# Kernel tuning notes

Measured on AMD Instinct MI355X. Metric: run time of the kernel, lower is better.

## Reference

```python
import jax, jax.numpy as jnp
import numpy as np

N_NODES = 100000
N_EDGES = 1600000
IN_DIM = 512
HID = 64
OUT_DIM = 5


def _gcn_conv(x, row, col, w, W, b, n_nodes):
    """PyG GCNConv: h = x @ W; out[col] += norm * h[row]; out += b.
    norm = deg^-1/2[row] * w * deg^-1/2[col], deg from edge weights scattered on col,
    with self-loops (weight 1) already appended by caller."""
    h = x @ W  # [N, F_out]
    deg = jax.ops.segment_sum(w, col, num_segments=n_nodes)  # [N]
    dinv = jnp.where(deg > 0, jax.lax.rsqrt(deg), 0.0)
    norm = dinv[row] * w * dinv[col]  # [E']
    msg = h[row] * norm[:, None]  # [E', F_out] edge-wise gather + scale
    out = jax.ops.segment_sum(msg, col, num_segments=n_nodes)  # scatter-add
    return out + b


def setup_inputs() -> dict:
    key = jax.random.key(0)
    ks = jax.random.split(key, 10)
    x = jax.random.normal(ks[0], (N_NODES, IN_DIM), dtype=jnp.float32)
    edge_index = jax.random.randint(ks[1], (2, N_EDGES), 0, N_NODES, dtype=jnp.int32)
    edge_attr = jax.random.uniform(ks[2], (N_EDGES,), dtype=jnp.float32)
    # Glorot-ish init for params
    W1 = jax.random.normal(ks[3], (IN_DIM, HID), dtype=jnp.float32) * (1.0 / np.sqrt(IN_DIM))
    b1 = jnp.zeros((HID,), dtype=jnp.float32)
    W2 = jax.random.normal(ks[4], (HID, HID), dtype=jnp.float32) * (1.0 / np.sqrt(HID))
    b2 = jnp.zeros((HID,), dtype=jnp.float32)
    Wfc = jax.random.normal(ks[5], (HID, OUT_DIM), dtype=jnp.float32) * (1.0 / np.sqrt(HID))
    bfc = jnp.zeros((OUT_DIM,), dtype=jnp.float32)
    return {"x": x, "edge_index": edge_index, "edge_attr": edge_attr,
            "W1": W1, "b1": b1, "W2": W2, "b2": b2, "Wfc": Wfc, "bfc": bfc}


def reference(x, edge_index, edge_attr, W1, b1, W2, b2, Wfc, bfc):
    n = x.shape[0]
    loop = jnp.arange(n, dtype=edge_index.dtype)
    row = jnp.concatenate([edge_index[0], loop])  # source nodes + self-loops
    col = jnp.concatenate([edge_index[1], loop])  # target nodes + self-loops
    w = jnp.concatenate([edge_attr, jnp.ones((n,), dtype=edge_attr.dtype)])
    h = jax.nn.relu(_gcn_conv(x, row, col, w, W1, b1, n))
    # dropout(p=0.5) is identity in eval/reference mode
    h = jax.nn.relu(_gcn_conv(h, row, col, w, W2, b2, n))
    return h @ Wfc + bfc
```

## Files before the change

kernel.cpp:

```cpp
#include <hip/hip_runtime.h>

#define HID 64
#define OUTD 5
#define BCAP 16384
#define PART_CHUNK 4096
#define CSTRIDE 16

typedef __attribute__((ext_vector_type(8))) short bf16x8;
typedef __attribute__((ext_vector_type(4))) float f32x4;

__device__ inline void split_bf16(float x, short& hi, short& lo) {
    unsigned u = __float_as_uint(x);
    unsigned h = u >> 16;
    float hf = __uint_as_float(h << 16);
    float lof = x - hf;
    unsigned l = __float_as_uint(lof) >> 16;
    hi = (short)h; lo = (short)l;
}

__device__ inline ushort f2bf(float x) {
    unsigned u = __float_as_uint(x);
    u += 0x7fffu + ((u >> 16) & 1u);
    return (ushort)(u >> 16);
}

__global__ void k_prep(const float* __restrict__ W1, const float* __restrict__ W2,
                       short* __restrict__ w1hi, short* __restrict__ w1lo,
                       short* __restrict__ w2hi, short* __restrict__ w2lo,
                       int* __restrict__ gcursor, int nbuck,
                       int* __restrict__ binCnt, int* __restrict__ binCur) {
    int gid = blockIdx.x * blockDim.x + threadIdx.x;
    if (gid < nbuck) gcursor[gid * CSTRIDE] = 0;
    if (gid < 64) { binCnt[gid * CSTRIDE] = 0; binCur[gid * CSTRIDE] = 0; }
    if (gid >= 32768 + 4096) return;
    int which = (gid >= 32768);
    int g = which ? gid - 32768 : gid;
    const float* W = which ? W2 : W1;
    short* ph = which ? w2hi : w1hi;
    short* pl = which ? w2lo : w1lo;
    int b = g & 7, lane = (g >> 3) & 63, c = (g >> 9) & 3, s = g >> 11;
    int k = s * 32 + 8 * (lane >> 4) + b;
    int j = c * 16 + (lane & 15);
    float x = W[k * 64 + j];
    short hi, lo; split_bf16(x, hi, lo);
    ph[g] = hi; pl[g] = lo;
}

__device__ inline void gemm1_body(const float* __restrict__ A,
                                  const short* __restrict__ whi,
                                  const short* __restrict__ wlo,
                                  ushort* __restrict__ C, int M, int bid, int tid) {
    const int K = 512, NS = 16;
    int lane = tid & 63;
    int wave = tid >> 6;
    int r0 = bid * 128 + wave * 32;

    int ar0 = r0 + (lane & 15);      if (ar0 >= M) ar0 = M - 1;
    int ar1 = r0 + 16 + (lane & 15); if (ar1 >= M) ar1 = M - 1;
    const float* pa0 = A + (size_t)ar0 * K + 8 * (lane >> 4);
    const float* pa1 = A + (size_t)ar1 * K + 8 * (lane >> 4);
    const bf16x8* bh = (const bf16x8*)whi + lane;
    const bf16x8* bl = (const bf16x8*)wlo + lane;

    f32x4 acc[2][4];
    #pragma unroll
    for (int r = 0; r < 2; r++)
        #pragma unroll
        for (int c = 0; c < 4; c++) acc[r][c] = (f32x4){0.f, 0.f, 0.f, 0.f};

    #pragma unroll
    for (int s = 0; s < NS; s++) {
        float4 x0 = *(const float4*)(pa0 + s * 32);
        float4 x1 = *(const float4*)(pa0 + s * 32 + 4);
        float4 y0 = *(const float4*)(pa1 + s * 32);
        float4 y1 = *(const float4*)(pa1 + s * 32 + 4);
        float xs[8] = {x0.x, x0.y, x0.z, x0.w, x1.x, x1.y, x1.z, x1.w};
        float ys[8] = {y0.x, y0.y, y0.z, y0.w, y1.x, y1.y, y1.z, y1.w};
        bf16x8 ah0, al0, ah1, al1;
        #pragma unroll
        for (int e = 0; e < 8; e++) {
            short h, l;
            split_bf16(xs[e], h, l); ah0[e] = h; al0[e] = l;
            split_bf16(ys[e], h, l); ah1[e] = h; al1[e] = l;
        }
        #pragma unroll
        for (int c = 0; c < 4; c++) {
            bf16x8 wh = bh[(s * 4 + c) * 64];
            bf16x8 wl = bl[(s * 4 + c) * 64];
            acc[0][c] = __builtin_amdgcn_mfma_f32_16x16x32_bf16(ah0, wh, acc[0][c], 0, 0, 0);
            acc[0][c] = __builtin_amdgcn_mfma_f32_16x16x32_bf16(ah0, wl, acc[0][c], 0, 0, 0);
            acc[0][c] = __builtin_amdgcn_mfma_f32_16x16x32_bf16(al0, wh, acc[0][c], 0, 0, 0);
            acc[1][c] = __builtin_amdgcn_mfma_f32_16x16x32_bf16(ah1, wh, acc[1][c], 0, 0, 0);
            acc[1][c] = __builtin_amdgcn_mfma_f32_16x16x32_bf16(ah1, wl, acc[1][c], 0, 0, 0);
            acc[1][c] = __builtin_amdgcn_mfma_f32_16x16x32_bf16(al1, wh, acc[1][c], 0, 0, 0);
        }
    }

    #pragma unroll
    for (int r = 0; r < 2; r++) {
        #pragma unroll
        for (int reg = 0; reg < 4; reg++) {
            int grow = r0 + r * 16 + 4 * (lane >> 4) + reg;
            if (grow < M) {
                #pragma unroll
                for (int c = 0; c < 4; c++)
                    C[(size_t)grow * 64 + c * 16 + (lane & 15)] = f2bf(acc[r][c][reg]);
            }
        }
    }
}

__global__ __launch_bounds__(256) void k_fused1(const float* __restrict__ x,
                                                const short* __restrict__ w1hi,
                                                const short* __restrict__ w1lo,
                                                ushort* __restrict__ h1, int M, int gGemm,
                                                const int* __restrict__ row,
                                                const int* __restrict__ col,
                                                const float* __restrict__ ea,
                                                int* __restrict__ gcursor,
                                                int2* __restrict__ bucket_mem,
                                                int nbuck, int E) {
    __shared__ int sh[512];
    int bid = blockIdx.x;
    int t = threadIdx.x;
    if (bid < gGemm) {
        gemm1_body(x, w1hi, w1lo, h1, M, bid, t);
        return;
    }
    int* hist = sh;
    int* basearr = sh + 256;
    int e0 = (bid - gGemm) * PART_CHUNK;
    if (t < nbuck) hist[t] = 0;
    __syncthreads();
    int cols[PART_CHUNK / 256];
    #pragma unroll
    for (int i = 0; i < PART_CHUNK / 256; i++) {
        int e = e0 + t + i * 256;
        cols[i] = (e < E) ? col[e] : -1;
        if (cols[i] >= 0) atomicAdd(&hist[cols[i] >> 9], 1);
    }
    __syncthreads();
    if (t < nbuck) {
        basearr[t] = atomicAdd(&gcursor[t * CSTRIDE], hist[t]);
        hist[t] = 0;
    }
    __syncthreads();
    #pragma unroll
    for (int i = 0; i < PART_CHUNK / 256; i++) {
        int e = e0 + t + i * 256;
        if (e < E) {
            int c = cols[i];
            int b = c >> 9;
            int pos = basearr[b] + atomicAdd(&hist[b], 1);
            if (pos < BCAP) {
                int pack = ((c & 511) << 17) | row[e];
                bucket_mem[(size_t)b * BCAP + pos] = make_int2(pack, __float_as_int(ea[e]));
            }
        }
    }
}

__global__ __launch_bounds__(256) void k_build(const int* __restrict__ gcursor,
                                               const int2* __restrict__ bucket_mem,
                                               int2* __restrict__ edges,
                                               int2* __restrict__ nodemeta,
                                               float* __restrict__ dinv,
                                               int* __restrict__ used,
                                               int* __restrict__ binCnt, int n) {
    __shared__ int hcnt[512];
    __shared__ int hoff[512];
    __shared__ float hdeg[512];
    __shared__ int ps[256];
    __shared__ int hbin[64];
    int b = blockIdx.x;
    int t = threadIdx.x;
    int cntb = gcursor[b * CSTRIDE]; if (cntb > BCAP) cntb = BCAP;
    const int2* bm = bucket_mem + (size_t)b * BCAP;

    #pragma unroll
    for (int l = t; l < 512; l += 256) { hcnt[l] = 0; hdeg[l] = 0.f; }
    if (t < 64) hbin[t] = 0;
    __syncthreads();
    for (int i = t; i < cntb; i += 256) atomicAdd(&hcnt[bm[i].x >> 17], 1);
    __syncthreads();
    int c0 = hcnt[2 * t], c1 = hcnt[2 * t + 1];
    int q0 = (c0 + 15) & ~15; if (q0 < 16) q0 = 16;
    int q1 = (c1 + 15) & ~15; if (q1 < 16) q1 = 16;
    ps[t] = q0 + q1;
    __syncthreads();
    for (int o = 1; o < 256; o <<= 1) {
        int v = (t >= o) ? ps[t - o] : 0;
        __syncthreads();
        ps[t] += v;
        __syncthreads();
    }
    int excl = ps[t] - (q0 + q1);
    hoff[2 * t] = excl;
    hoff[2 * t + 1] = excl + q0;
    if (t == 255) used[b] = ps[255];
    __syncthreads();
    #pragma unroll
    for (int l = t; l < 512; l += 256) hcnt[l] = 0;
    __syncthreads();
    for (int i = t; i < cntb; i += 256) {
        int2 eM = bm[i];
        int local = eM.x >> 17;
        int src = eM.x & 0x1FFFF;
        int p = hoff[local] + atomicAdd(&hcnt[local], 1);
        edges[(size_t)b * BCAP + p] = make_int2(src, eM.y);
        atomicAdd(&hdeg[local], __int_as_float(eM.y));
    }
    __syncthreads();
    #pragma unroll
    for (int l = t; l < 512; l += 256) {
        int node = b * 512 + l;
        if (node < n) {
            int cnt = hcnt[l];
            int pc = (cnt + 15) & ~15; if (pc < 16) pc = 16;
            for (int p2 = cnt; p2 < pc; p2++)
                edges[(size_t)b * BCAP + hoff[l] + p2] = make_int2(node, 0);
            nodemeta[node] = make_int2(b * BCAP + hoff[l], pc);
            dinv[node] = rsqrtf(hdeg[l] + 1.0f);
            int bin = pc >> 4; if (bin > 63) bin = 63;
            atomicAdd(&hbin[bin], 1);
        }
    }
    __syncthreads();
    if (t < 64 && hbin[t] > 0) atomicAdd(&binCnt[t * CSTRIDE], hbin[t]);
}

__global__ void k_norm2(int2* __restrict__ edges, const float* __restrict__ dinv,
                        const int* __restrict__ used, int n, int nbuck, int gNorm,
                        const int* __restrict__ binCnt, int* __restrict__ binBase) {
    if (blockIdx.x == (unsigned)gNorm) {
        if (threadIdx.x == 0) {
            int acc = 0;
            for (int i = 0; i < 64; i++) { binBase[i] = acc; acc += binCnt[i * CSTRIDE]; }
        }
        return;
    }
    int gid = blockIdx.x * blockDim.x + threadIdx.x;
    int b = gid >> 14;
    if (b >= nbuck) return;
    int slot = gid & (BCAP - 1);
    if (slot >= used[b]) return;
    size_t idx = (size_t)b * BCAP + slot;
    int2 c = edges[idx];
    if ((unsigned)c.x < (unsigned)n) {
        c.y = __float_as_int(dinv[c.x] * __int_as_float(c.y));
        edges[idx] = c;
    }
}

__global__ void k_scatter(const int2* __restrict__ nodemeta, const int* __restrict__ binBase,
                          int* __restrict__ binCur, int* __restrict__ perm, int n) {
    __shared__ int lh[64];
    __shared__ int gb[64];
    int t = threadIdx.x;
    if (t < 64) lh[t] = 0;
    __syncthreads();
    int i = blockIdx.x * 256 + t;
    int bin = 0, r = 0;
    bool v = (i < n);
    if (v) {
        int pc = nodemeta[i].y;
        bin = pc >> 4; if (bin > 63) bin = 63;
        r = atomicAdd(&lh[bin], 1);
    }
    __syncthreads();
    if (t < 64) gb[t] = (lh[t] > 0) ? atomicAdd(&binCur[t * CSTRIDE], lh[t]) : 0;
    __syncthreads();
    if (v) perm[binBase[bin] + gb[bin] + r] = i;
}

template<int FC>
__global__ void k_gather4(const ushort* __restrict__ h, const int2* __restrict__ nodemeta,
                          const int2* __restrict__ edges, const float* __restrict__ dinv,
                          const int* __restrict__ perm,
                          const float* __restrict__ bias, const float* __restrict__ Wfc,
                          const float* __restrict__ bfc, ushort* __restrict__ outb,
                          float* __restrict__ outf, int n) {
    int gw = (blockIdx.x * blockDim.x + threadIdx.x) >> 6;
    int lane = threadIdx.x & 63;
    int s = lane & 15;
    int idx = gw * 4 + (lane >> 4);
    bool valid = (idx < n);
    if (!valid) idx = n - 1;
    int node = perm[idx];

    int2 meta = nodemeta[node];
    int cnt = meta.y;
    const int2* seg = edges + meta.x;
    uint2 self_u = *(const uint2*)&h[(size_t)node * 64 + 4 * s];
    float dvc = dinv[node];
    int mc = max(cnt, __shfl_xor(cnt, 16));
    mc = max(mc, __shfl_xor(mc, 32));

    float a0 = 0.f, a1 = 0.f, a2 = 0.f, a3 = 0.f;
    for (int i = 0; i < mc; i += 16) {
        int base = (i < cnt) ? i : (cnt - 16);
        float live = (i < cnt) ? 1.f : 0.f;
        int4 m[8];
        #pragma unroll
        for (int q = 0; q < 8; q++) m[q] = *(const int4*)(seg + base + 2 * q);
        uint2 v[16];
        #pragma unroll
        for (int q = 0; q < 8; q++) {
            v[2 * q]     = *(const uint2*)&h[(size_t)m[q].x * 64 + 4 * s];
            v[2 * q + 1] = *(const uint2*)&h[(size_t)m[q].z * 64 + 4 * s];
        }
        #pragma unroll
        for (int q = 0; q < 8; q++) {
            float w0 = __int_as_float(m[q].y) * live;
            float w1 = __int_as_float(m[q].w) * live;
            uint2 va = v[2 * q], vb = v[2 * q + 1];
            a0 += w0 * __uint_as_float(va.x << 16);
            a1 += w0 * __uint_as_float(va.x & 0xffff0000u);
            a2 += w0 * __uint_as_float(va.y << 16);
            a3 += w0 * __uint_as_float(va.y & 0xffff0000u);
            a0 += w1 * __uint_as_float(vb.x << 16);
            a1 += w1 * __uint_as_float(vb.x & 0xffff0000u);
            a2 += w1 * __uint_as_float(vb.y << 16);
            a3 += w1 * __uint_as_float(vb.y & 0xffff0000u);
        }
    }

    float4 bv = *(const float4*)&bias[4 * s];
    float dd = dvc * dvc;
    float r0 = fmaxf(dvc * a0 + dd * __uint_as_float(self_u.x << 16) + bv.x, 0.f);
    float r1 = fmaxf(dvc * a1 + dd * __uint_as_float(self_u.x & 0xffff0000u) + bv.y, 0.f);
    float r2 = fmaxf(dvc * a2 + dd * __uint_as_float(self_u.y << 16) + bv.z, 0.f);
    float r3 = fmaxf(dvc * a3 + dd * __uint_as_float(self_u.y & 0xffff0000u) + bv.w, 0.f);

    if (FC == 0) {
        if (valid) {
            uint lo = ((uint)f2bf(r1) << 16) | (uint)f2bf(r0);
            uint hi = ((uint)f2bf(r3) << 16) | (uint)f2bf(r2);
            *(uint2*)&outb[(size_t)node * 64 + 4 * s] = make_uint2(lo, hi);
        }
    } else {
        #pragma unroll
        for (int j = 0; j < OUTD; j++) {
            float p = r0 * Wfc[(4 * s) * OUTD + j] + r1 * Wfc[(4 * s + 1) * OUTD + j]
                    + r2 * Wfc[(4 * s + 2) * OUTD + j] + r3 * Wfc[(4 * s + 3) * OUTD + j];
            #pragma unroll
            for (int o = 1; o <= 8; o <<= 1) p += __shfl_xor(p, o);
            if (s == j && valid) outf[(size_t)node * OUTD + j] = p + bfc[j];
        }
    }
}

__global__ __launch_bounds__(256) void k_gemm2(const ushort* __restrict__ A,
                                               const short* __restrict__ whi,
                                               const short* __restrict__ wlo,
                                               ushort* __restrict__ C, int M) {
    int tid = threadIdx.x;
    int lane = tid & 63;
    int wave = tid >> 6;
    int r0 = blockIdx.x * 128 + wave * 32;

    int ar0 = r0 + (lane & 15);      if (ar0 >= M) ar0 = M - 1;
    int ar1 = r0 + 16 + (lane & 15); if (ar1 >= M) ar1 = M - 1;
    const ushort* pa0 = A + (size_t)ar0 * 64 + 8 * (lane >> 4);
    const ushort* pa1 = A + (size_t)ar1 * 64 + 8 * (lane >> 4);
    const bf16x8* bh = (const bf16x8*)whi + lane;
    const bf16x8* bl = (const bf16x8*)wlo + lane;

    f32x4 acc[2][4];
    #pragma unroll
    for (int r = 0; r < 2; r++)
        #pragma unroll
        for (int c = 0; c < 4; c++) acc[r][c] = (f32x4){0.f, 0.f, 0.f, 0.f};

    #pragma unroll
    for (int s = 0; s < 2; s++) {
        bf16x8 a0 = *(const bf16x8*)(pa0 + s * 32);
        bf16x8 a1 = *(const bf16x8*)(pa1 + s * 32);
        #pragma unroll
        for (int c = 0; c < 4; c++) {
            bf16x8 wh = bh[(s * 4 + c) * 64];
            bf16x8 wl = bl[(s * 4 + c) * 64];
            acc[0][c] = __builtin_amdgcn_mfma_f32_16x16x32_bf16(a0, wh, acc[0][c], 0, 0, 0);
            acc[0][c] = __builtin_amdgcn_mfma_f32_16x16x32_bf16(a0, wl, acc[0][c], 0, 0, 0);
            acc[1][c] = __builtin_amdgcn_mfma_f32_16x16x32_bf16(a1, wh, acc[1][c], 0, 0, 0);
            acc[1][c] = __builtin_amdgcn_mfma_f32_16x16x32_bf16(a1, wl, acc[1][c], 0, 0, 0);
        }
    }

    #pragma unroll
    for (int r = 0; r < 2; r++) {
        #pragma unroll
        for (int reg = 0; reg < 4; reg++) {
            int grow = r0 + r * 16 + 4 * (lane >> 4) + reg;
            if (grow < M) {
                #pragma unroll
                for (int c = 0; c < 4; c++)
                    C[(size_t)grow * 64 + c * 16 + (lane & 15)] = f2bf(acc[r][c][reg]);
            }
        }
    }
}

extern "C" void kernel_launch(void* const* d_in, const int* in_sizes, int n_in,
                              void* d_out, int out_size, void* d_ws, size_t ws_size,
                              hipStream_t stream) {
    const float* x   = (const float*)d_in[0];
    const int*   ei  = (const int*)d_in[1];
    const float* ea  = (const float*)d_in[2];
    const float* W1  = (const float*)d_in[3];
    const float* b1  = (const float*)d_in[4];
    const float* W2  = (const float*)d_in[5];
    const float* b2  = (const float*)d_in[6];
    const float* Wfc = (const float*)d_in[7];
    const float* bfc = (const float*)d_in[8];

    const int N = in_sizes[0] / 512;
    const int E = in_sizes[1] / 2;
    const int nbuck = (N + 511) >> 9;

    const int* row = ei;
    const int* col = ei + E;

    uintptr_t p = (uintptr_t)d_ws;
    auto carve = [&](size_t bytes) -> void* {
        void* r = (void*)p;
        p += (bytes + 255) & ~(size_t)255;
        return r;
    };
    int*    gcursor    = (int*)carve((size_t)nbuck * CSTRIDE * 4);
    int*    used       = (int*)carve((size_t)nbuck * 4);
    int*    binCnt     = (int*)carve(64 * CSTRIDE * 4);
    int*    binCur     = (int*)carve(64 * CSTRIDE * 4);
    int*    binBase    = (int*)carve(64 * 4);
    int*    perm       = (int*)carve((size_t)N * 4);
    float*  dinv       = (float*)carve((size_t)N * 4);
    int2*   nodemeta   = (int2*)carve((size_t)N * 8);
    int2*   bucket_mem = (int2*)carve((size_t)nbuck * BCAP * 8);
    int2*   edges      = (int2*)carve((size_t)nbuck * BCAP * 8);
    short*  w1hi       = (short*)carve(32768 * 2);
    short*  w1lo       = (short*)carve(32768 * 2);
    short*  w2hi       = (short*)carve(4096 * 2);
    short*  w2lo       = (short*)carve(4096 * 2);
    ushort* hbuf       = (ushort*)carve((size_t)N * 64 * 2);
    ushort* abuf       = (ushort*)carve((size_t)N * 64 * 2);
    (void)ws_size;

    const int B = 256;
    int gGemm = (N + 127) / 128;
    int gPart = (E + PART_CHUNK - 1) / PART_CHUNK;
    int gNorm = nbuck * (BCAP / B);
    int gGath = (((N + 3) / 4) * 64 + B - 1) / B;
    int gScat = (N + B - 1) / B;
    int gPrep = (32768 + 4096 + B - 1) / B;

    k_prep<<<gPrep, B, 0, stream>>>(W1, W2, w1hi, w1lo, w2hi, w2lo,
                                    gcursor, nbuck, binCnt, binCur);
    k_fused1<<<gGemm + gPart, B, 0, stream>>>(x, w1hi, w1lo, hbuf, N, gGemm,
                                              row, col, ea, gcursor, bucket_mem, nbuck, E);
    k_build<<<nbuck, B, 0, stream>>>(gcursor, bucket_mem, edges, nodemeta,
                                     dinv, used, binCnt, N);
    k_norm2<<<gNorm + 1, B, 0, stream>>>(edges, dinv, used, N, nbuck, gNorm,
                                         binCnt, binBase);
    k_scatter<<<gScat, B, 0, stream>>>(nodemeta, binBase, binCur, perm, N);
    k_gather4<0><<<gGath, B, 0, stream>>>(hbuf, nodemeta, edges, dinv, perm, b1,
                                          nullptr, nullptr, abuf, nullptr, N);
    k_gemm2<<<gGemm, B, 0, stream>>>(abuf, w2hi, w2lo, hbuf, N);
    k_gather4<1><<<gGath, B, 0, stream>>>(hbuf, nodemeta, edges, dinv, perm, b2,
                                          Wfc, bfc, nullptr, (float*)d_out, N);
}
```

Baseline: 239.6 us.

## Stage GEMM1 A tiles through swizzled LDS with coalesced loads

Replaces the per-lane strided global float4 loads of x in the first GEMM with cooperative, coalesced loads of a 128x32 tile into LDS, using an XOR swizzle to avoid bank conflicts. Each wave then reads its MFMA operands from LDS. The aim is better global memory coalescing on the dominant 200MB read of x. The cost is two barriers per K-step with no double buffering, which serializes load and compute and may hurt latency hiding. The shared buffer is enlarged and reused for the partition histogram.

```diff
diff --git a/kernel.cpp b/kernel.cpp
--- a/kernel.cpp
+++ b/kernel.cpp
@@ -49,16 +49,13 @@
 __device__ inline void gemm1_body(const float* __restrict__ A,
                                   const short* __restrict__ whi,
                                   const short* __restrict__ wlo,
-                                  ushort* __restrict__ C, int M, int bid, int tid) {
-    const int K = 512, NS = 16;
+                                  ushort* __restrict__ C, int M, int bid, int tid,
+                                  float* __restrict__ As) {
+    const int K = 512;
     int lane = tid & 63;
     int wave = tid >> 6;
-    int r0 = bid * 128 + wave * 32;
-
-    int ar0 = r0 + (lane & 15);      if (ar0 >= M) ar0 = M - 1;
-    int ar1 = r0 + 16 + (lane & 15); if (ar1 >= M) ar1 = M - 1;
-    const float* pa0 = A + (size_t)ar0 * K + 8 * (lane >> 4);
-    const float* pa1 = A + (size_t)ar1 * K + 8 * (lane >> 4);
+    int r0 = bid * 128;
+
     const bf16x8* bh = (const bf16x8*)whi + lane;
     const bf16x8* bl = (const bf16x8*)wlo + lane;
 
@@ -68,12 +65,27 @@
         #pragma unroll
         for (int c = 0; c < 4; c++) acc[r][c] = (f32x4){0.f, 0.f, 0.f, 0.f};
 
-    #pragma unroll
-    for (int s = 0; s < NS; s++) {
-        float4 x0 = *(const float4*)(pa0 + s * 32);
-        float4 x1 = *(const float4*)(pa0 + s * 32 + 4);
-        float4 y0 = *(const float4*)(pa1 + s * 32);
-        float4 y1 = *(const float4*)(pa1 + s * 32 + 4);
+    int lr0 = wave * 32 + (lane & 15);
+    int lr1 = lr0 + 16;
+    int cb = 2 * (lane >> 4);
+
+    for (int s = 0; s < 16; s++) {
+        int k0 = s * 32;
+        __syncthreads();
+        #pragma unroll
+        for (int i = 0; i < 4; i++) {
+            int sl = i * 256 + tid;
+            int row = sl >> 3, c4 = sl & 7;
+            int gr = r0 + row; if (gr >= M) gr = M - 1;
+            float4 v = *(const float4*)(A + (size_t)gr * K + k0 + c4 * 4);
+            *(float4*)&As[(size_t)(row * 8 + (c4 ^ (row & 7))) * 4] = v;
+        }
+        __syncthreads();
+
+        float4 x0 = *(const float4*)&As[(size_t)(lr0 * 8 + ((cb)     ^ (lr0 & 7))) * 4];
+        float4 x1 = *(const float4*)&As[(size_t)(lr0 * 8 + ((cb + 1) ^ (lr0 & 7))) * 4];
+        float4 y0 = *(const float4*)&As[(size_t)(lr1 * 8 + ((cb)     ^ (lr1 & 7))) * 4];
+        float4 y1 = *(const float4*)&As[(size_t)(lr1 * 8 + ((cb + 1) ^ (lr1 & 7))) * 4];
         float xs[8] = {x0.x, x0.y, x0.z, x0.w, x1.x, x1.y, x1.z, x1.w};
         float ys[8] = {y0.x, y0.y, y0.z, y0.w, y1.x, y1.y, y1.z, y1.w};
         bf16x8 ah0, al0, ah1, al1;
@@ -96,11 +108,12 @@
         }
     }
 
+    int wr0 = r0 + wave * 32;
     #pragma unroll
     for (int r = 0; r < 2; r++) {
         #pragma unroll
         for (int reg = 0; reg < 4; reg++) {
-            int grow = r0 + r * 16 + 4 * (lane >> 4) + reg;
+            int grow = wr0 + r * 16 + 4 * (lane >> 4) + reg;
             if (grow < M) {
                 #pragma unroll
                 for (int c = 0; c < 4; c++)
@@ -120,15 +133,15 @@
                                                 int* __restrict__ gcursor,
                                                 int2* __restrict__ bucket_mem,
                                                 int nbuck, int E) {
-    __shared__ int sh[512];
+    __shared__ __align__(16) char ldsbuf[128 * 32 * 4];
     int bid = blockIdx.x;
     int t = threadIdx.x;
     if (bid < gGemm) {
-        gemm1_body(x, w1hi, w1lo, h1, M, bid, t);
+        gemm1_body(x, w1hi, w1lo, h1, M, bid, t, (float*)ldsbuf);
         return;
     }
-    int* hist = sh;
-    int* basearr = sh + 256;
+    int* hist = (int*)ldsbuf;
+    int* basearr = (int*)ldsbuf + 256;
     int e0 = (bid - gGemm) * PART_CHUNK;
     if (t < nbuck) hist[t] = 0;
     __syncthreads();
```

Measured after the change: 230.8 us, median of 2. 3.7% less time.
